# Kernel optimization log

Measured on AMD Instinct MI355X. Metric: run time of the kernel, lower is better.

The kernel has to match this reference:

```python
import jax, jax.numpy as jnp
import numpy as np

D_MODEL = 1024
N_HEADS = 16
DEPTH = D_MODEL // N_HEADS  # 64
BATCH, SEQ = 4, 2048


def setup_inputs() -> dict:
    key = jax.random.key(0)
    ks = jax.random.split(key, 8)
    x = jax.random.normal(ks[0], (BATCH, SEQ, D_MODEL), dtype=jnp.float32)
    # Per-head Dense(depth) weights stacked over heads: [H, d_model, depth]
    s = 1.0 / np.sqrt(D_MODEL)
    Wq = jax.random.normal(ks[1], (N_HEADS, D_MODEL, DEPTH), dtype=jnp.float32) * s
    Wk = jax.random.normal(ks[2], (N_HEADS, D_MODEL, DEPTH), dtype=jnp.float32) * s
    Wv = jax.random.normal(ks[3], (N_HEADS, D_MODEL, DEPTH), dtype=jnp.float32) * s
    bq = jnp.zeros((N_HEADS, DEPTH), dtype=jnp.float32)
    bk = jnp.zeros((N_HEADS, DEPTH), dtype=jnp.float32)
    bv = jnp.zeros((N_HEADS, DEPTH), dtype=jnp.float32)
    Wo = jax.random.normal(ks[4], (D_MODEL, D_MODEL), dtype=jnp.float32) * s
    bo = jnp.zeros((D_MODEL,), dtype=jnp.float32)
    return {"x": x, "Wq": Wq, "bq": bq, "Wk": Wk, "bk": bk,
            "Wv": Wv, "bv": bv, "Wo": Wo, "bo": bo}


def reference(x, Wq, bq, Wk, bk, Wv, bv, Wo, bo):
    # Per-head projections, batched over heads: [b, h, s, depth]
    q = jnp.einsum('bsd,hde->bhse', x, Wq) + bq[None, :, None, :]
    k = jnp.einsum('bsd,hde->bhse', x, Wk) + bk[None, :, None, :]
    v = jnp.einsum('bsd,hde->bhse', x, Wv) + bv[None, :, None, :]
    scale = 1.0 / jnp.sqrt(jnp.float32(DEPTH))
    scores = jnp.einsum('bhqe,bhke->bhqk', q, k) * scale  # [b, h, s, s]
    attn = jax.nn.softmax(scores, axis=-1)
    z = jnp.einsum('bhqk,bhke->bhqe', attn, v)  # [b, h, s, depth]
    # Concat heads along last axis (head-major order matches tf.concat of per-head outputs)
    multi_head = z.transpose(0, 2, 1, 3).reshape(BATCH, SEQ, D_MODEL)
    return multi_head @ Wo + bo
```

## Files before the change

### kernel.cpp

```cpp
#include <hip/hip_runtime.h>

typedef unsigned short u16;
typedef __bf16 bf16x8 __attribute__((ext_vector_type(8)));
typedef float f32x4 __attribute__((ext_vector_type(4)));
typedef float f32x16 __attribute__((ext_vector_type(16)));
typedef unsigned int u32x4 __attribute__((ext_vector_type(4)));
typedef unsigned int u32x2 __attribute__((ext_vector_type(2)));

__device__ __forceinline__ u16 f2b(float f) {
  union { float f; unsigned u; } v; v.f = f;
  return (u16)((v.u + 0x7fffu + ((v.u >> 16) & 1u)) >> 16);
}

__device__ __forceinline__ unsigned pkbf(float a, float b) {
#if __has_builtin(__builtin_amdgcn_cvt_pk_bf16_f32)
  typedef __bf16 bf16x2v __attribute__((ext_vector_type(2)));
  bf16x2v r = __builtin_amdgcn_cvt_pk_bf16_f32(a, b);
  return __builtin_bit_cast(unsigned, r);
#else
  return (unsigned)f2b(a) | ((unsigned)f2b(b) << 16);
#endif
}

__device__ __forceinline__ float fexp2(float x) {
#if __has_builtin(__builtin_amdgcn_exp2f)
  return __builtin_amdgcn_exp2f(x);
#else
  return exp2f(x);
#endif
}

__device__ __forceinline__ bf16x8 ldfrag(const u16* p) {
  u32x4 r = *(const u32x4*)p;
  return __builtin_bit_cast(bf16x8, r);
}

#define GLOAD_LDS16(gp, lp)                                                        \
  __builtin_amdgcn_global_load_lds((const __attribute__((address_space(1))) void*)(gp), \
                                   (__attribute__((address_space(3))) void*)(lp), 16, 0, 0)

#define MFMA16(a, b, c) __builtin_amdgcn_mfma_f32_16x16x32_bf16((a), (b), (c), 0, 0, 0)
#define MFMA32(a, b, c) __builtin_amdgcn_mfma_f32_32x32x16_bf16((a), (b), (c), 0, 0, 0)

#define QSC 0.18033688011f


__global__ __launch_bounds__(256) void k_pack_x(const float* __restrict__ x,
                                                u16* __restrict__ xb) {
  int i = (blockIdx.x * 256 + threadIdx.x) * 4;
  float4 v = *(const float4*)(x + i);
  u32x2 o;
  o[0] = pkbf(v.x, v.y);
  o[1] = pkbf(v.z, v.w);
  *(u32x2*)(xb + i) = o;
}

__global__ __launch_bounds__(256) void k_pack_w(const float* __restrict__ Wq,
                                                const float* __restrict__ Wk,
                                                const float* __restrict__ Wv,
                                                u16* __restrict__ wt) {
  __shared__ u16 tile[64][65];
  int bid = blockIdx.x;
  int p = bid >> 8, rem = bid & 255, h = rem >> 4, dt = rem & 15;
  const float* W = (p == 0) ? Wq : (p == 1) ? Wk : Wv;
  int tid = threadIdx.x;
  for (int i = tid; i < 4096; i += 256) {
    int d = i >> 6, e = i & 63;
    tile[e][d] = f2b(W[h * 65536 + (dt * 64 + d) * 64 + e]);
  }
  __syncthreads();
  for (int i = tid; i < 4096; i += 256) {
    int e = i >> 6, d = i & 63;
    wt[(size_t)(p * 1024 + h * 64 + e) * 1024 + dt * 64 + d] = tile[e][d];
  }
}

__global__ __launch_bounds__(256) void k_pack_wo(const float* __restrict__ Wo,
                                                 u16* __restrict__ wt) {
  __shared__ u16 tile[64][65];
  int kt = blockIdx.x >> 4, nt = blockIdx.x & 15;
  int tid = threadIdx.x;
  for (int i = tid; i < 4096; i += 256) {
    int dk = i >> 6, de = i & 63;
    tile[de][dk] = f2b(Wo[(size_t)(kt * 64 + dk) * 1024 + nt * 64 + de]);
  }
  __syncthreads();
  for (int i = tid; i < 4096; i += 256) {
    int de = i >> 6, dk = i & 63;
    wt[(size_t)(nt * 64 + de) * 1024 + kt * 64 + dk] = tile[de][dk];
  }
}


__device__ __forceinline__ void gemm_core(const u16* __restrict__ A, const u16* __restrict__ Bt,
                                          int row0, int col0, u16* As, u16* Bs, f32x4 acc[4][4]) {
  const int tid = threadIdx.x, w = tid >> 6, lane = tid & 63;
  const int quad = lane >> 4, l15 = lane & 15;
  const int wm = (w >> 1) * 64, wn = (w & 1) * 64;
  for (int k0 = 0; k0 < 1024; k0 += 32) {
#pragma unroll
    for (int i = 0; i < 2; i++) {
      int bse = (w * 2 + i) * 512;
      int flat = bse + lane * 8;
      int r = flat >> 5, c = flat & 31;
      GLOAD_LDS16(A + (size_t)(row0 + r) * 1024 + k0 + c, As + bse);
      GLOAD_LDS16(Bt + (size_t)(col0 + r) * 1024 + k0 + c, Bs + bse);
    }
    __syncthreads();
    bf16x8 af[4], bfr[4];
#pragma unroll
    for (int t = 0; t < 4; t++) {
      af[t] = ldfrag(As + (wm + t * 16 + l15) * 32 + quad * 8);
      bfr[t] = ldfrag(Bs + (wn + t * 16 + l15) * 32 + quad * 8);
    }
#pragma unroll
    for (int mt = 0; mt < 4; mt++)
#pragma unroll
      for (int nt = 0; nt < 4; nt++)
        acc[mt][nt] = MFMA16(af[mt], bfr[nt], acc[mt][nt]);
    __syncthreads();
  }
}


__global__ __launch_bounds__(256) void k_gemm_qkv(const u16* __restrict__ xb, const u16* __restrict__ wt,
                                                  const float* __restrict__ bq, const float* __restrict__ bk,
                                                  const float* __restrict__ bv,
                                                  u16* __restrict__ qo, u16* __restrict__ ko,
                                                  u16* __restrict__ vto) {
  __shared__ u16 As[4096], Bs[4096];
  f32x4 acc[4][4];
  const f32x4 z4 = {0.f, 0.f, 0.f, 0.f};
#pragma unroll
  for (int a = 0; a < 4; a++)
#pragma unroll
    for (int b = 0; b < 4; b++) acc[a][b] = z4;
  const int row0 = blockIdx.x * 128, col0 = blockIdx.y * 128;
  gemm_core(xb, wt, row0, col0, As, Bs, acc);
  const int tid = threadIdx.x, w = tid >> 6, lane = tid & 63;
  const int quad = lane >> 4, l15 = lane & 15;
  const int wm = (w >> 1) * 64, wn = (w & 1) * 64;
#pragma unroll
  for (int nt = 0; nt < 4; nt++) {
    int c = col0 + wn + nt * 16 + l15;
    int p = c >> 10, rem = c & 1023;
    int h = rem >> 6, e = rem & 63;
    const float* bias = (p == 0) ? bq : (p == 1) ? bk : bv;
    float bval = bias[rem];
#pragma unroll
    for (int mt = 0; mt < 4; mt++) {
#pragma unroll
      for (int reg = 0; reg < 4; reg++) {
        int r = row0 + wm + mt * 16 + quad * 4 + reg;
        int b_ = r >> 11, s = r & 2047;
        int bh = b_ * 16 + h;
        float val = acc[mt][nt][reg] + bval;
        if (p == 0) {
          qo[((size_t)bh * 2048 + s) * 64 + e] = f2b(val * QSC);
        } else if (p == 1) {
          ko[((size_t)bh * 2048 + s) * 64 + e] = f2b(val);
        } else {
          vto[((size_t)bh * 64 + e) * 2048 + s] = f2b(val);
        }
      }
    }
  }
}


__global__ __launch_bounds__(256) void k_gemm_out(const u16* __restrict__ zb, const u16* __restrict__ wt,
                                                  const float* __restrict__ bo, float* __restrict__ out) {
  __shared__ u16 As[4096], Bs[4096];
  f32x4 acc[4][4];
  const f32x4 z4 = {0.f, 0.f, 0.f, 0.f};
#pragma unroll
  for (int a = 0; a < 4; a++)
#pragma unroll
    for (int b = 0; b < 4; b++) acc[a][b] = z4;
  const int row0 = blockIdx.x * 128, col0 = blockIdx.y * 128;
  gemm_core(zb, wt, row0, col0, As, Bs, acc);
  const int tid = threadIdx.x, w = tid >> 6, lane = tid & 63;
  const int quad = lane >> 4, l15 = lane & 15;
  const int wm = (w >> 1) * 64, wn = (w & 1) * 64;
#pragma unroll
  for (int nt = 0; nt < 4; nt++) {
    int c = col0 + wn + nt * 16 + l15;
    float bval = bo[c];
#pragma unroll
    for (int mt = 0; mt < 4; mt++) {
#pragma unroll
      for (int reg = 0; reg < 4; reg++) {
        int r = row0 + wm + mt * 16 + quad * 4 + reg;
        out[(size_t)r * 1024 + c] = acc[mt][nt][reg] + bval;
      }
    }
  }
}


__global__ __launch_bounds__(256) void k_attn(const u16* __restrict__ q, const u16* __restrict__ k,
                                              const u16* __restrict__ vt, u16* __restrict__ z) {
  __shared__ u16 Ks[64 * 72], Vs[64 * 72], Ps[4][32 * 72];
  const int tid = threadIdx.x, w = tid >> 6, lane = tid & 63;
  const int l31 = lane & 31, hi = lane >> 5;
  const int bh = blockIdx.y, s0 = blockIdx.x * 128;
  const size_t base = (size_t)bh * 2048 * 64;
  const int qrow = s0 + w * 32 + l31;

  bf16x8 qf[4];
  {
    const u16* qp = q + base + (size_t)qrow * 64 + hi * 8;
#pragma unroll
    for (int ks = 0; ks < 4; ks++) qf[ks] = ldfrag(qp + ks * 16);
  }

  f32x16 accT[2], lvec;
#pragma unroll
  for (int r = 0; r < 16; r++) { accT[0][r] = 0.f; accT[1][r] = 0.f; lvec[r] = 0.f; }

  const int srow = tid >> 3;
  const int scol = (tid & 7) * 8;
  const u16* kg = k + base;
  const u16* vg = vt + base;

  u32x4 kr0, kr1, vr0, vr1;
  kr0 = *(const u32x4*)(kg + (size_t)srow * 64 + scol);
  kr1 = *(const u32x4*)(kg + (size_t)(srow + 32) * 64 + scol);
  vr0 = *(const u32x4*)(vg + (size_t)srow * 2048 + scol);
  vr1 = *(const u32x4*)(vg + (size_t)(srow + 32) * 2048 + scol);

  u16* Pw = Ps[w];
  const int poff = l31 * 72;

  for (int kc = 0; kc < 2048; kc += 64) {
    __syncthreads();
    *(u32x4*)&Ks[srow * 72 + scol] = kr0;
    *(u32x4*)&Ks[(srow + 32) * 72 + scol] = kr1;
    *(u32x4*)&Vs[srow * 72 + scol] = vr0;
    *(u32x4*)&Vs[(srow + 32) * 72 + scol] = vr1;
    __syncthreads();
    if (kc + 64 < 2048) {
      int kn = kc + 64;
      kr0 = *(const u32x4*)(kg + (size_t)(kn + srow) * 64 + scol);
      kr1 = *(const u32x4*)(kg + (size_t)(kn + srow + 32) * 64 + scol);
      vr0 = *(const u32x4*)(vg + (size_t)srow * 2048 + kn + scol);
      vr1 = *(const u32x4*)(vg + (size_t)(srow + 32) * 2048 + kn + scol);
    }

    f32x16 sc[2];
#pragma unroll
    for (int t = 0; t < 2; t++) {
#pragma unroll
      for (int r = 0; r < 16; r++) sc[t][r] = 0.f;
#pragma unroll
      for (int ks = 0; ks < 4; ks++) {
        bf16x8 kf = ldfrag(&Ks[(t * 32 + l31) * 72 + ks * 16 + hi * 8]);
        sc[t] = MFMA32(kf, qf[ks], sc[t]);
      }
    }

#pragma unroll
    for (int t = 0; t < 2; t++)
#pragma unroll
      for (int r = 0; r < 16; r++) sc[t][r] = fexp2(sc[t][r]);
    lvec += sc[0];
    lvec += sc[1];

#pragma unroll
    for (int t = 0; t < 2; t++)
#pragma unroll
      for (int r4 = 0; r4 < 4; r4++) {
        u32x2 d;
        d[0] = pkbf(sc[t][r4 * 4 + 0], sc[t][r4 * 4 + 1]);
        d[1] = pkbf(sc[t][r4 * 4 + 2], sc[t][r4 * 4 + 3]);
        *(u32x2*)&Pw[poff + t * 32 + r4 * 8 + hi * 4] = d;
      }

#pragma unroll
    for (int ks = 0; ks < 4; ks++) {
      bf16x8 pf = ldfrag(&Pw[poff + ks * 16 + hi * 8]);
#pragma unroll
      for (int et = 0; et < 2; et++) {
        bf16x8 vf = ldfrag(&Vs[(et * 32 + l31) * 72 + ks * 16 + hi * 8]);
        accT[et] = MFMA32(vf, pf, accT[et]);
      }
    }
  }

  float l = 0.f;
#pragma unroll
  for (int r = 0; r < 16; r++) l += lvec[r];
  l += __shfl_xor(l, 32);
  float inv = 1.f / l;

  const int b_ = bh >> 4, h = bh & 15;
  u16* zr = z + ((size_t)(b_ * 2048 + qrow)) * 1024 + h * 64;
#pragma unroll
  for (int et = 0; et < 2; et++)
#pragma unroll
    for (int rr = 0; rr < 16; rr += 2) {
      unsigned pkd = pkbf(accT[et][rr] * inv, accT[et][rr + 1] * inv);
      int e = et * 32 + (rr & 3) + 8 * (rr >> 2) + 4 * hi;
      *(unsigned*)&zr[e] = pkd;
    }
}


extern "C" void kernel_launch(void* const* d_in, const int* in_sizes, int n_in,
                              void* d_out, int out_size, void* d_ws, size_t ws_size,
                              hipStream_t stream) {
  (void)in_sizes; (void)n_in; (void)out_size;
  const float* x  = (const float*)d_in[0];
  const float* Wq = (const float*)d_in[1];
  const float* bq = (const float*)d_in[2];
  const float* Wk = (const float*)d_in[3];
  const float* bk = (const float*)d_in[4];
  const float* Wv = (const float*)d_in[5];
  const float* bv = (const float*)d_in[6];
  const float* Wo = (const float*)d_in[7];
  const float* bo = (const float*)d_in[8];
  float* out = (float*)d_out;
  char* ws = (char*)d_ws;
  if (ws_size < 92274688u) return;

  u16* xb   = (u16*)(ws + 0);
  u16* wqkv = (u16*)(ws + 16777216);
  u16* wo_t = (u16*)(ws + 23068672);
  u16* qb   = (u16*)(ws + 25165824);
  u16* kb   = (u16*)(ws + 41943040);
  u16* vtb  = (u16*)(ws + 58720256);
  u16* zb   = (u16*)(ws + 75497472);

  k_pack_x<<<8192, 256, 0, stream>>>(x, xb);
  k_pack_w<<<768, 256, 0, stream>>>(Wq, Wk, Wv, wqkv);
  k_pack_wo<<<256, 256, 0, stream>>>(Wo, wo_t);
  k_gemm_qkv<<<dim3(64, 24), 256, 0, stream>>>(xb, wqkv, bq, bk, bv, qb, kb, vtb);
  k_attn<<<dim3(16, 64), 256, 0, stream>>>(qb, kb, vtb, zb);
  k_gemm_out<<<dim3(64, 8), 256, 0, stream>>>(zb, wo_t, bo, out);
}
```

Measured before the change: 322.6 us.

## Switch projection GEMMs to 32x32 MFMA and merge pack kernels into one launch

Replaces the 16x16x32 MFMA tiling in the QKV and output GEMMs with 32x32x16 MFMA tiles, so fewer instructions and fragment loads are issued per k-step. For V, the A and B operands are swapped so each lane holds consecutive sequence positions, which is meant to make the transposed V^T stores coalesced. The three pre-pack kernels become one launch, and x packing now handles 8 elements per thread. The tradeoffs are a different register footprint and new index math in the GEMM epilogues.

```diff
diff --git a/kernel.cpp b/kernel.cpp
--- a/kernel.cpp
+++ b/kernel.cpp
@@ -39,63 +39,67 @@
   __builtin_amdgcn_global_load_lds((const __attribute__((address_space(1))) void*)(gp), \
                                    (__attribute__((address_space(3))) void*)(lp), 16, 0, 0)
 
-#define MFMA16(a, b, c) __builtin_amdgcn_mfma_f32_16x16x32_bf16((a), (b), (c), 0, 0, 0)
 #define MFMA32(a, b, c) __builtin_amdgcn_mfma_f32_32x32x16_bf16((a), (b), (c), 0, 0, 0)
 
 #define QSC 0.18033688011f
 
 
-__global__ __launch_bounds__(256) void k_pack_x(const float* __restrict__ x,
-                                                u16* __restrict__ xb) {
-  int i = (blockIdx.x * 256 + threadIdx.x) * 4;
-  float4 v = *(const float4*)(x + i);
-  u32x2 o;
-  o[0] = pkbf(v.x, v.y);
-  o[1] = pkbf(v.z, v.w);
-  *(u32x2*)(xb + i) = o;
-}
-
-__global__ __launch_bounds__(256) void k_pack_w(const float* __restrict__ Wq,
-                                                const float* __restrict__ Wk,
-                                                const float* __restrict__ Wv,
-                                                u16* __restrict__ wt) {
+__global__ __launch_bounds__(256) void k_pack(const float* __restrict__ x,
+                                              const float* __restrict__ Wq,
+                                              const float* __restrict__ Wk,
+                                              const float* __restrict__ Wv,
+                                              const float* __restrict__ Wo,
+                                              u16* __restrict__ xb,
+                                              u16* __restrict__ wqkv,
+                                              u16* __restrict__ wo_t) {
+  const int bid = blockIdx.x, tid = threadIdx.x;
+  if (bid < 4096) {
+    int i = (bid * 256 + tid) * 8;
+    float4 v0 = *(const float4*)(x + i);
+    float4 v1 = *(const float4*)(x + i + 4);
+    u32x4 o;
+    o[0] = pkbf(v0.x, v0.y);
+    o[1] = pkbf(v0.z, v0.w);
+    o[2] = pkbf(v1.x, v1.y);
+    o[3] = pkbf(v1.z, v1.w);
+    *(u32x4*)(xb + i) = o;
+    return;
+  }
   __shared__ u16 tile[64][65];
-  int bid = blockIdx.x;
-  int p = bid >> 8, rem = bid & 255, h = rem >> 4, dt = rem & 15;
-  const float* W = (p == 0) ? Wq : (p == 1) ? Wk : Wv;
-  int tid = threadIdx.x;
-  for (int i = tid; i < 4096; i += 256) {
-    int d = i >> 6, e = i & 63;
-    tile[e][d] = f2b(W[h * 65536 + (dt * 64 + d) * 64 + e]);
-  }
-  __syncthreads();
-  for (int i = tid; i < 4096; i += 256) {
-    int e = i >> 6, d = i & 63;
-    wt[(size_t)(p * 1024 + h * 64 + e) * 1024 + dt * 64 + d] = tile[e][d];
-  }
-}
-
-__global__ __launch_bounds__(256) void k_pack_wo(const float* __restrict__ Wo,
-                                                 u16* __restrict__ wt) {
-  __shared__ u16 tile[64][65];
-  int kt = blockIdx.x >> 4, nt = blockIdx.x & 15;
-  int tid = threadIdx.x;
-  for (int i = tid; i < 4096; i += 256) {
-    int dk = i >> 6, de = i & 63;
-    tile[de][dk] = f2b(Wo[(size_t)(kt * 64 + dk) * 1024 + nt * 64 + de]);
-  }
-  __syncthreads();
-  for (int i = tid; i < 4096; i += 256) {
-    int de = i >> 6, dk = i & 63;
-    wt[(size_t)(nt * 64 + de) * 1024 + kt * 64 + dk] = tile[de][dk];
-  }
-}
-
-
-__device__ __forceinline__ void gemm_core(const u16* __restrict__ A, const u16* __restrict__ Bt,
-                                          int row0, int col0, u16* As, u16* Bs, f32x4 acc[4][4]) {
+  if (bid < 4864) {
+    int b2 = bid - 4096;
+    int p = b2 >> 8, rem = b2 & 255, h = rem >> 4, dt = rem & 15;
+    const float* W = (p == 0) ? Wq : (p == 1) ? Wk : Wv;
+    for (int i = tid; i < 4096; i += 256) {
+      int d = i >> 6, e = i & 63;
+      tile[e][d] = f2b(W[h * 65536 + (dt * 64 + d) * 64 + e]);
+    }
+    __syncthreads();
+    for (int i = tid; i < 4096; i += 256) {
+      int e = i >> 6, d = i & 63;
+      wqkv[(size_t)(p * 1024 + h * 64 + e) * 1024 + dt * 64 + d] = tile[e][d];
+    }
+  } else {
+    int b2 = bid - 4864;
+    int kt = b2 >> 4, nt = b2 & 15;
+    for (int i = tid; i < 4096; i += 256) {
+      int dk = i >> 6, de = i & 63;
+      tile[de][dk] = f2b(Wo[(size_t)(kt * 64 + dk) * 1024 + nt * 64 + de]);
+    }
+    __syncthreads();
+    for (int i = tid; i < 4096; i += 256) {
+      int de = i >> 6, dk = i & 63;
+      wo_t[(size_t)(nt * 64 + de) * 1024 + kt * 64 + dk] = tile[de][dk];
+    }
+  }
+}
+
+
+template <bool SWAP>
+__device__ __forceinline__ void gemm_core32(const u16* __restrict__ A, const u16* __restrict__ Bt,
+                                            int row0, int col0, u16* As, u16* Bs, f32x16 acc[2][2]) {
   const int tid = threadIdx.x, w = tid >> 6, lane = tid & 63;
-  const int quad = lane >> 4, l15 = lane & 15;
+  const int l31 = lane & 31, hi = lane >> 5;
   const int wm = (w >> 1) * 64, wn = (w & 1) * 64;
   for (int k0 = 0; k0 < 1024; k0 += 32) {
 #pragma unroll
@@ -107,17 +111,22 @@
       GLOAD_LDS16(Bt + (size_t)(col0 + r) * 1024 + k0 + c, Bs + bse);
     }
     __syncthreads();
-    bf16x8 af[4], bfr[4];
-#pragma unroll
-    for (int t = 0; t < 4; t++) {
-      af[t] = ldfrag(As + (wm + t * 16 + l15) * 32 + quad * 8);
-      bfr[t] = ldfrag(Bs + (wn + t * 16 + l15) * 32 + quad * 8);
-    }
-#pragma unroll
-    for (int mt = 0; mt < 4; mt++)
-#pragma unroll
-      for (int nt = 0; nt < 4; nt++)
-        acc[mt][nt] = MFMA16(af[mt], bfr[nt], acc[mt][nt]);
+    bf16x8 af[2][2], bfr[2][2];
+#pragma unroll
+    for (int t = 0; t < 2; t++)
+#pragma unroll
+      for (int s = 0; s < 2; s++) {
+        af[t][s] = ldfrag(As + (wm + t * 32 + l31) * 32 + s * 16 + hi * 8);
+        bfr[t][s] = ldfrag(Bs + (wn + t * 32 + l31) * 32 + s * 16 + hi * 8);
+      }
+#pragma unroll
+    for (int mt = 0; mt < 2; mt++)
+#pragma unroll
+      for (int nt = 0; nt < 2; nt++)
+#pragma unroll
+        for (int s = 0; s < 2; s++)
+          acc[mt][nt] = SWAP ? MFMA32(bfr[nt][s], af[mt][s], acc[mt][nt])
+                             : MFMA32(af[mt][s], bfr[nt][s], acc[mt][nt]);
     __syncthreads();
   }
 }
@@ -129,38 +138,64 @@
                                                   u16* __restrict__ qo, u16* __restrict__ ko,
                                                   u16* __restrict__ vto) {
   __shared__ u16 As[4096], Bs[4096];
-  f32x4 acc[4][4];
-  const f32x4 z4 = {0.f, 0.f, 0.f, 0.f};
-#pragma unroll
-  for (int a = 0; a < 4; a++)
-#pragma unroll
-    for (int b = 0; b < 4; b++) acc[a][b] = z4;
+  f32x16 acc[2][2];
+#pragma unroll
+  for (int a = 0; a < 2; a++)
+#pragma unroll
+    for (int b = 0; b < 2; b++)
+#pragma unroll
+      for (int r = 0; r < 16; r++) acc[a][b][r] = 0.f;
+
   const int row0 = blockIdx.x * 128, col0 = blockIdx.y * 128;
-  gemm_core(xb, wt, row0, col0, As, Bs, acc);
+  const int p = blockIdx.y >> 3;
+  const int colr = (blockIdx.y & 7) * 128;
   const int tid = threadIdx.x, w = tid >> 6, lane = tid & 63;
-  const int quad = lane >> 4, l15 = lane & 15;
+  const int l31 = lane & 31, hi = lane >> 5;
   const int wm = (w >> 1) * 64, wn = (w & 1) * 64;
-#pragma unroll
-  for (int nt = 0; nt < 4; nt++) {
-    int c = col0 + wn + nt * 16 + l15;
-    int p = c >> 10, rem = c & 1023;
-    int h = rem >> 6, e = rem & 63;
-    const float* bias = (p == 0) ? bq : (p == 1) ? bk : bv;
-    float bval = bias[rem];
-#pragma unroll
-    for (int mt = 0; mt < 4; mt++) {
-#pragma unroll
-      for (int reg = 0; reg < 4; reg++) {
-        int r = row0 + wm + mt * 16 + quad * 4 + reg;
-        int b_ = r >> 11, s = r & 2047;
-        int bh = b_ * 16 + h;
-        float val = acc[mt][nt][reg] + bval;
-        if (p == 0) {
-          qo[((size_t)bh * 2048 + s) * 64 + e] = f2b(val * QSC);
-        } else if (p == 1) {
-          ko[((size_t)bh * 2048 + s) * 64 + e] = f2b(val);
-        } else {
-          vto[((size_t)bh * 64 + e) * 2048 + s] = f2b(val);
+
+  if (p == 2) {
+    gemm_core32<true>(xb, wt, row0, col0, As, Bs, acc);
+#pragma unroll
+    for (int mt = 0; mt < 2; mt++) {
+      int rb = row0 + wm + mt * 32;
+      int b_ = rb >> 11;
+      int s_ = (rb & 2047) + l31;
+#pragma unroll
+      for (int nt = 0; nt < 2; nt++) {
+        int ebase = colr + wn + nt * 32;
+#pragma unroll
+        for (int g = 0; g < 4; g++) {
+          float4 bvv = *(const float4*)(bv + ebase + g * 8 + hi * 4);
+#pragma unroll
+          for (int j = 0; j < 4; j++) {
+            int rem = ebase + g * 8 + hi * 4 + j;
+            int h = rem >> 6, e = rem & 63;
+            float val = acc[mt][nt][g * 4 + j] + (&bvv.x)[j];
+            vto[(((size_t)(b_ * 16 + h)) * 64 + e) * 2048 + s_] = f2b(val);
+          }
+        }
+      }
+    }
+  } else {
+    gemm_core32<false>(xb, wt, row0, col0, As, Bs, acc);
+    u16* dst = (p == 0) ? qo : ko;
+    const float* bias = (p == 0) ? bq : bk;
+    const float qsc = (p == 0) ? QSC : 1.0f;
+#pragma unroll
+    for (int nt = 0; nt < 2; nt++) {
+      int rem = colr + wn + nt * 32 + l31;
+      int h = rem >> 6, e = rem & 63;
+      float bval = bias[rem];
+#pragma unroll
+      for (int mt = 0; mt < 2; mt++) {
+        int rb = row0 + wm + mt * 32;
+        int b_ = rb >> 11, sb = rb & 2047;
+        size_t obase = ((size_t)(b_ * 16 + h) * 2048) * 64 + e;
+#pragma unroll
+        for (int reg = 0; reg < 16; reg++) {
+          int s_ = sb + (reg & 3) + 8 * (reg >> 2) + 4 * hi;
+          float val = (acc[mt][nt][reg] + bval) * qsc;
+          dst[obase + (size_t)s_ * 64] = f2b(val);
         }
       }
     }
@@ -171,26 +206,30 @@
 __global__ __launch_bounds__(256) void k_gemm_out(const u16* __restrict__ zb, const u16* __restrict__ wt,
                                                   const float* __restrict__ bo, float* __restrict__ out) {
   __shared__ u16 As[4096], Bs[4096];
-  f32x4 acc[4][4];
-  const f32x4 z4 = {0.f, 0.f, 0.f, 0.f};
-#pragma unroll
-  for (int a = 0; a < 4; a++)
-#pragma unroll
-    for (int b = 0; b < 4; b++) acc[a][b] = z4;
+  f32x16 acc[2][2];
+#pragma unroll
+  for (int a = 0; a < 2; a++)
+#pragma unroll
+    for (int b = 0; b < 2; b++)
+#pragma unroll
+      for (int r = 0; r < 16; r++) acc[a][b][r] = 0.f;
+
   const int row0 = blockIdx.x * 128, col0 = blockIdx.y * 128;
-  gemm_core(zb, wt, row0, col0, As, Bs, acc);
+  gemm_core32<false>(zb, wt, row0, col0, As, Bs, acc);
+
   const int tid = threadIdx.x, w = tid >> 6, lane = tid & 63;
-  const int quad = lane >> 4, l15 = lane & 15;
+  const int l31 = lane & 31, hi = lane >> 5;
   const int wm = (w >> 1) * 64, wn = (w & 1) * 64;
 #pragma unroll
-  for (int nt = 0; nt < 4; nt++) {
-    int c = col0 + wn + nt * 16 + l15;
+  for (int nt = 0; nt < 2; nt++) {
+    int c = col0 + wn + nt * 32 + l31;
     float bval = bo[c];
 #pragma unroll
-    for (int mt = 0; mt < 4; mt++) {
-#pragma unroll
-      for (int reg = 0; reg < 4; reg++) {
-        int r = row0 + wm + mt * 16 + quad * 4 + reg;
+    for (int mt = 0; mt < 2; mt++) {
+      int rb = row0 + wm + mt * 32;
+#pragma unroll
+      for (int reg = 0; reg < 16; reg++) {
+        int r = rb + (reg & 3) + 8 * (reg >> 2) + 4 * hi;
         out[(size_t)r * 1024 + c] = acc[mt][nt][reg] + bval;
       }
     }
@@ -331,9 +370,7 @@
   u16* vtb  = (u16*)(ws + 58720256);
   u16* zb   = (u16*)(ws + 75497472);
 
-  k_pack_x<<<8192, 256, 0, stream>>>(x, xb);
-  k_pack_w<<<768, 256, 0, stream>>>(Wq, Wk, Wv, wqkv);
-  k_pack_wo<<<256, 256, 0, stream>>>(Wo, wo_t);
+  k_pack<<<5120, 256, 0, stream>>>(x, Wq, Wk, Wv, Wo, xb, wqkv, wo_t);
   k_gemm_qkv<<<dim3(64, 24), 256, 0, stream>>>(xb, wqkv, bq, bk, bv, qb, kb, vtb);
   k_attn<<<dim3(16, 64), 256, 0, stream>>>(qb, kb, vtb, zb);
   k_gemm_out<<<dim3(64, 8), 256, 0, stream>>>(zb, wo_t, bo, out);
```

New measurement: 315.0 us. -2.3%, faster.
